# Optimization experiments

Measured on AMD Instinct MI355X. Metric: run time of the kernel, lower is better.

The kernel has to match this reference:

```python
import jax, jax.numpy as jnp
import numpy as np

N0 = 50000
N1 = 50000
E = 500000
IN_DIM = 128
OUT_DIM = 128
H = 8
DK = OUT_DIM // H  # 16
SQRT_DK = float(np.sqrt(DK))
NUM_TYPES = 2
NUM_REL = 3
# relations: (src_type, dst_type, e_id)
RELATIONS = [(0, 1, 0), (1, 0, 1), (0, 0, 2)]


def setup_inputs() -> dict:
    key = jax.random.key(0)
    ks = jax.random.split(key, 24)
    d = {}
    d["h0"] = jax.random.normal(ks[0], (N0, IN_DIM), dtype=jnp.float32)
    d["h1"] = jax.random.normal(ks[1], (N1, IN_DIM), dtype=jnp.float32)
    d["src0"] = jax.random.randint(ks[2], (E,), 0, N0)
    d["dst0"] = jax.random.randint(ks[3], (E,), 0, N1)
    d["src1"] = jax.random.randint(ks[4], (E,), 0, N1)
    d["dst1"] = jax.random.randint(ks[5], (E,), 0, N0)
    d["src2"] = jax.random.randint(ks[6], (E,), 0, N0)
    d["dst2"] = jax.random.randint(ks[7], (E,), 0, N0)
    w_scale = 1.0 / np.sqrt(IN_DIM)
    # per-node-type stacked linear weights (k, q, v, a), torch Linear convention: y = x @ W.T + b
    d["Wk"] = jax.random.normal(ks[8], (NUM_TYPES, OUT_DIM, IN_DIM), dtype=jnp.float32) * w_scale
    d["bk"] = jnp.zeros((NUM_TYPES, OUT_DIM), dtype=jnp.float32)
    d["Wq"] = jax.random.normal(ks[9], (NUM_TYPES, OUT_DIM, IN_DIM), dtype=jnp.float32) * w_scale
    d["bq"] = jnp.zeros((NUM_TYPES, OUT_DIM), dtype=jnp.float32)
    d["Wv"] = jax.random.normal(ks[10], (NUM_TYPES, OUT_DIM, IN_DIM), dtype=jnp.float32) * w_scale
    d["bv"] = jnp.zeros((NUM_TYPES, OUT_DIM), dtype=jnp.float32)
    d["Wa"] = jax.random.normal(ks[11], (NUM_TYPES, OUT_DIM, OUT_DIM), dtype=jnp.float32) * w_scale
    d["ba"] = jnp.zeros((NUM_TYPES, OUT_DIM), dtype=jnp.float32)
    xavier = float(np.sqrt(6.0 / (DK + DK)))
    d["rel_att"] = jax.random.uniform(ks[12], (NUM_REL, H, DK, DK), dtype=jnp.float32, minval=-xavier, maxval=xavier)
    d["rel_msg"] = jax.random.uniform(ks[13], (NUM_REL, H, DK, DK), dtype=jnp.float32, minval=-xavier, maxval=xavier)
    d["rel_pri"] = jnp.ones((NUM_REL, H), dtype=jnp.float32)
    d["skip"] = jnp.ones((NUM_TYPES,), dtype=jnp.float32)
    return d


def _lin(x, W, b):
    return x @ W.T + b


def reference(h0, h1, src0, dst0, src1, dst1, src2, dst2,
              Wk, bk, Wq, bq, Wv, bv, Wa, ba,
              rel_att, rel_msg, rel_pri, skip):
    h = [h0, h1]
    edges = [(src0, dst0), (src1, dst1), (src2, dst2)]
    # per-type projections, reshaped to (N, H, DK)
    k = [_lin(h[t], Wk[t], bk[t]).reshape(-1, H, DK) for t in range(NUM_TYPES)]
    q = [_lin(h[t], Wq[t], bq[t]).reshape(-1, H, DK) for t in range(NUM_TYPES)]
    v = [_lin(h[t], Wv[t], bv[t]).reshape(-1, H, DK) for t in range(NUM_TYPES)]

    agg = [[] for _ in range(NUM_TYPES)]
    for (s, dt, e), (src, dst) in zip(RELATIONS, edges):
        # relation-specific transforms of source k and v
        kr = jnp.einsum('nhi,hij->nhj', k[s], rel_att[e])
        vr = jnp.einsum('nhi,hij->nhj', v[s], rel_msg[e])
        # per-edge dot-product score (E, H)
        score = (q[dt][dst] * kr[src]).sum(-1) * rel_pri[e] / SQRT_DK
        n_dst = h[dt].shape[0]
        # edge softmax normalized by dst (stable)
        m = jax.ops.segment_max(score, dst, num_segments=n_dst)
        ex = jnp.exp(score - m[dst])
        den = jax.ops.segment_sum(ex, dst, num_segments=n_dst)
        attn = ex / den[dst]  # (E, H)
        # weighted message scatter-sum -> (n_dst, H, DK)
        msg = vr[src] * attn[:, :, None]
        agg[dt].append(jax.ops.segment_sum(msg, dst, num_segments=n_dst))

    new_h = []
    for t in range(NUM_TYPES):
        # cross_reducer='mean' over relations targeting this node type
        tmean = sum(agg[t]) / float(len(agg[t]))
        tflat = tmean.reshape(-1, OUT_DIM)
        trans = _lin(tflat, Wa[t], ba[t])  # dropout = identity (eval)
        alpha = jax.nn.sigmoid(skip[t])
        new_h.append(trans * alpha + h[t] * (1.0 - alpha))
    return tuple(new_h)
```

## Files before the change

### kernel.cpp

```cpp
#include <hip/hip_runtime.h>

typedef __attribute__((ext_vector_type(8))) _Float16 half8;
typedef __attribute__((ext_vector_type(2))) _Float16 half2v;
typedef __attribute__((ext_vector_type(4))) float f32x4;

#define NB 196
#define CHK 2048
#define CAPB 4096
#define PSTRIDE 6144

__device__ __forceinline__ unsigned short f2h(float f) {
  _Float16 h = (_Float16)f;
  return __builtin_bit_cast(unsigned short, h);
}
__device__ __forceinline__ float fdot2(unsigned a, unsigned b, float c) {
  return __builtin_amdgcn_fdot2(__builtin_bit_cast(half2v, a), __builtin_bit_cast(half2v, b), c,
                                false);
}

#define DPPADD(v, ctrl) \
  ((v) + __int_as_float(__builtin_amdgcn_update_dpp(0, __float_as_int(v), ctrl, 0xF, 0xF, true)))

__global__ void cvt2_kernel(const float* __restrict__ a, unsigned short* __restrict__ oa,
                            const float* __restrict__ b, unsigned short* __restrict__ ob,
                            int n8, unsigned short* __restrict__ z0,
                            unsigned short* __restrict__ z1, unsigned short* __restrict__ z2) {
  int t = threadIdx.x;
  if (blockIdx.y == 2) {
    if (blockIdx.x == 0 && t < 192) {
      int r = t >> 6;
      unsigned short* z = r == 0 ? z0 : (r == 1 ? z1 : z2);
      ((uint2*)z)[t & 63] = make_uint2(0, 0);
    }
    return;
  }
  int i = blockIdx.x * 256 + t;
  if (i >= n8) return;
  const float* in = blockIdx.y ? b : a;
  unsigned short* out = blockIdx.y ? ob : oa;
  const float4* p = (const float4*)(in + (size_t)i * 8);
  float4 x = p[0], y = p[1];
  uint4 v;
  v.x = f2h(x.x) | ((unsigned)f2h(x.y) << 16);
  v.y = f2h(x.z) | ((unsigned)f2h(x.w) << 16);
  v.z = f2h(y.x) | ((unsigned)f2h(y.y) << 16);
  v.w = f2h(y.z) | ((unsigned)f2h(y.w) << 16);
  *(uint4*)(out + (size_t)i * 8) = v;
}

__global__ void compose_w_kernel(const float* __restrict__ Wk, const float* __restrict__ bk,
                                 const float* __restrict__ Wv, const float* __restrict__ bv,
                                 const float* __restrict__ rel_att, const float* __restrict__ rel_msg,
                                 const float* __restrict__ rel_pri,
                                 unsigned short* __restrict__ Wkr, float* __restrict__ bkr,
                                 unsigned short* __restrict__ Wvr, float* __restrict__ bvr) {
  int e = blockIdx.x;
  int o = blockIdx.y;
  int z = blockIdx.z;
  int c = threadIdx.x;
  int hd = o >> 4, j = o & 15;
  const int se[3] = {0, 1, 0};
  int s = se[e];
  const float* W = z ? Wv : Wk;
  const float* b = z ? bv : bk;
  const float* R = z ? rel_msg : rel_att;
  float scale = z ? 1.0f : (rel_pri[e * 8 + hd] * 0.25f);
  float acc = 0.0f, bacc = 0.0f;
#pragma unroll
  for (int i = 0; i < 16; ++i) {
    float r = R[((e * 8 + hd) * 16 + i) * 16 + j];
    acc += W[(s * 128 + hd * 16 + i) * 128 + c] * r;
    bacc += b[s * 128 + hd * 16 + i] * r;
  }
  unsigned short* Wo = z ? Wvr : Wkr;
  float* bo = z ? bvr : bkr;
  Wo[((size_t)e * 128 + o) * 128 + c] = f2h(acc * scale);
  if (c == 0) bo[e * 128 + o] = bacc * scale;
}

struct ProjFP {
  const float* A[2];
  int M[2];
  int nj[2];
  const unsigned short* W[10];
  const float* b[10];
  unsigned short* out[10];
  int ostr[10];
};

__global__ __launch_bounds__(256) void proj_gemm_fused(ProjFP P) {
  __shared__ short As[128 * 128];
  int type = blockIdx.y;
  const float* __restrict__ A = P.A[type];
  int M = P.M[type];
  int nj = P.nj[type];
  int base = type * 5;
  int row0 = blockIdx.x * 128;
  if (row0 >= M) return;
  int t = threadIdx.x;
  bool full = (row0 + 128 <= M);
#pragma unroll
  for (int it = 0; it < 8; ++it) {
    int o = (it * 256 + t) * 8;
    int row = o >> 7, col = o & 127;
    int gr = row0 + row;
    uint4 av = make_uint4(0, 0, 0, 0);
    if (full || gr < M) {
      float4 x = *(const float4*)(A + (size_t)gr * 128 + col);
      float4 y = *(const float4*)(A + (size_t)gr * 128 + col + 4);
      av.x = f2h(x.x) | ((unsigned)f2h(x.y) << 16);
      av.y = f2h(x.z) | ((unsigned)f2h(x.w) << 16);
      av.z = f2h(y.x) | ((unsigned)f2h(y.y) << 16);
      av.w = f2h(y.z) | ((unsigned)f2h(y.w) << 16);
    }
    int sw = o ^ ((row & 7) << 3);
    *(uint4*)(&As[sw]) = av;
  }
  __syncthreads();
  int wid = t >> 6, l = t & 63;
  int wr = wid >> 1, wc = wid & 1;
  int lr = l & 15, kb = l >> 4;
  for (int j = 0;; ++j) {
    const unsigned short* __restrict__ W = P.W[base + j];
    f32x4 acc[4][4] = {};
#pragma unroll
    for (int ks = 0; ks < 4; ++ks) {
      half8 af[4], bfr[4];
#pragma unroll
      for (int m = 0; m < 4; ++m) {
        int row = wr * 64 + m * 16 + lr;
        int h = (row * 128 + kb * 8 + ks * 32) ^ ((row & 7) << 3);
        af[m] = *(half8*)(&As[h]);
      }
#pragma unroll
      for (int n = 0; n < 4; ++n) {
        int row = wc * 64 + n * 16 + lr;
        bfr[n] = *(const half8*)(W + (size_t)row * 128 + kb * 8 + ks * 32);
      }
#pragma unroll
      for (int m = 0; m < 4; ++m)
#pragma unroll
        for (int n = 0; n < 4; ++n)
          acc[m][n] = __builtin_amdgcn_mfma_f32_16x16x32_f16(af[m], bfr[n], acc[m][n], 0, 0, 0);
    }
    const float* bias = P.b[base + j];
    unsigned short* out = P.out[base + j];
    int ostr = P.ostr[base + j];
    int rb = row0 + wr * 64 + (l >> 4) * 4;
#pragma unroll
    for (int m = 0; m < 4; ++m)
#pragma unroll
      for (int jr = 0; jr < 4; ++jr) {
        int grow = rb + m * 16 + jr;
        if (grow < M) {
#pragma unroll
          for (int n = 0; n < 4; ++n) {
            int col = wc * 64 + n * 16 + lr;
            out[(size_t)grow * ostr + col] = f2h(acc[m][n][jr] + bias[col]);
          }
        }
      }
    if (j + 1 >= nj) break;
  }
}

__global__ __launch_bounds__(256) void final_gemm_mfma(
    float* __restrict__ dout, const unsigned short* __restrict__ Tb0,
    const unsigned short* __restrict__ Tb1, const unsigned short* __restrict__ Wab,
    const float* __restrict__ ba, const float* __restrict__ h0, const float* __restrict__ h1,
    const float* __restrict__ skip, int N0, int N1) {
  __shared__ short As[128 * 128];
  int type = blockIdx.y;
  int M = type ? N1 : N0;
  const unsigned short* T = type ? Tb1 : Tb0;
  const unsigned short* W = Wab + (size_t)type * 16384;
  const float* bias = ba + type * 128;
  const float* h = type ? h1 : h0;
  float* O = dout + (type ? (size_t)N0 * 128 : 0);
  int row0 = blockIdx.x * 128;
  if (row0 >= M) return;
  int t = threadIdx.x;
  bool full = (row0 + 128 <= M);
#pragma unroll
  for (int it = 0; it < 8; ++it) {
    int o = (it * 256 + t) * 8;
    int row = o >> 7;
    int gr = row0 + row;
    uint4 av = make_uint4(0, 0, 0, 0);
    if (full || gr < M) av = *(const uint4*)(T + (size_t)gr * 128 + (o & 127));
    int sw = o ^ ((row & 7) << 3);
    *(uint4*)(&As[sw]) = av;
  }
  __syncthreads();
  int wid = t >> 6, l = t & 63;
  int wr = wid >> 1, wc = wid & 1;
  int lr = l & 15, kb = l >> 4;
  f32x4 acc[4][4] = {};
#pragma unroll
  for (int ks = 0; ks < 4; ++ks) {
    half8 af[4], bfr[4];
#pragma unroll
    for (int m = 0; m < 4; ++m) {
      int row = wr * 64 + m * 16 + lr;
      int h2 = (row * 128 + kb * 8 + ks * 32) ^ ((row & 7) << 3);
      af[m] = *(half8*)(&As[h2]);
    }
#pragma unroll
    for (int n = 0; n < 4; ++n) {
      int row = wc * 64 + n * 16 + lr;
      bfr[n] = *(const half8*)(W + (size_t)row * 128 + kb * 8 + ks * 32);
    }
#pragma unroll
    for (int m = 0; m < 4; ++m)
#pragma unroll
      for (int n = 0; n < 4; ++n)
        acc[m][n] = __builtin_amdgcn_mfma_f32_16x16x32_f16(af[m], bfr[n], acc[m][n], 0, 0, 0);
  }
  float alpha = 1.0f / (1.0f + __expf(-skip[type]));
  float beta = 1.0f - alpha;
  int rb = row0 + wr * 64 + (l >> 4) * 4;
#pragma unroll
  for (int m = 0; m < 4; ++m)
#pragma unroll
    for (int jr = 0; jr < 4; ++jr) {
      int grow = rb + m * 16 + jr;
      if (grow < M) {
#pragma unroll
        for (int n = 0; n < 4; ++n) {
          int col = wc * 64 + n * 16 + lr;
          float vout = alpha * (acc[m][n][jr] + bias[col]) + beta * h[(size_t)grow * 128 + col];
          O[(size_t)grow * 128 + col] = vout;
        }
      }
    }
}


__global__ __launch_bounds__(256) void bhist_kernel(const int* __restrict__ d0,
                                                    const int* __restrict__ d1,
                                                    const int* __restrict__ d2,
                                                    int* __restrict__ bh, int E) {
  __shared__ int lh[NB];
  int r = blockIdx.y;
  const int* dst = r == 0 ? d0 : (r == 1 ? d1 : d2);
  int t = threadIdx.x;
  int lo = blockIdx.x * CHK;
  int hi = lo + CHK < E ? lo + CHK : E;
  for (int j = t; j < NB; j += 256) lh[j] = 0;
  __syncthreads();
  for (int i = lo + t; i < hi; i += 256) atomicAdd(&lh[dst[i] >> 8], 1);
  __syncthreads();
  for (int j = t; j < NB; j += 256) {
    int v = lh[j];
    if (v) atomicAdd(&bh[r * NB + j], v);
  }
}

__global__ __launch_bounds__(256) void bin_kernel(
    const int* __restrict__ s0, const int* __restrict__ d0, const int* __restrict__ s1,
    const int* __restrict__ d1, const int* __restrict__ s2, const int* __restrict__ d2,
    const int* __restrict__ bh, int* __restrict__ bcur, unsigned* __restrict__ bo0,
    unsigned* __restrict__ bo1, unsigned* __restrict__ bo2, int E) {
  __shared__ unsigned st[CHK];
  __shared__ int ga[CHK];
  __shared__ int hist[NB];
  __shared__ int scn[256];
  __shared__ int gb[NB];
  __shared__ int bbl[NB];
  int r = blockIdx.y;
  const int* src = r == 0 ? s0 : (r == 1 ? s1 : s2);
  const int* dst = r == 0 ? d0 : (r == 1 ? d1 : d2);
  unsigned* bo = r == 0 ? bo0 : (r == 1 ? bo1 : bo2);
  int t = threadIdx.x;
  {
    int v0 = (t < NB) ? bh[r * NB + t] : 0;
    scn[t] = v0;
    __syncthreads();
    for (int off = 1; off < 256; off <<= 1) {
      int u = (t >= off) ? scn[t - off] : 0;
      __syncthreads();
      scn[t] += u;
      __syncthreads();
    }
    if (t < NB) bbl[t] = scn[t] - v0;
    __syncthreads();
  }
  int lo = blockIdx.x * CHK;
  int hi = lo + CHK < E ? lo + CHK : E;
  int nloc = hi - lo;
  if (nloc <= 0) return;
  for (int j = t; j < NB; j += 256) hist[j] = 0;
  __syncthreads();
  int myb[CHK / 256], myr[CHK / 256];
  unsigned mye[CHK / 256];
#pragma unroll
  for (int k = 0; k < CHK / 256; ++k) {
    int i = lo + k * 256 + t;
    myb[k] = -1;
    if (i < hi) {
      int d = dst[i];
      int b = d >> 8;
      mye[k] = (unsigned)src[i] | ((unsigned)d << 16);
      myb[k] = b;
      myr[k] = atomicAdd(&hist[b], 1);
    }
  }
  __syncthreads();
  int v = (t < NB) ? hist[t] : 0;
  scn[t] = v;
  __syncthreads();
  for (int off = 1; off < 256; off <<= 1) {
    int u = (t >= off) ? scn[t - off] : 0;
    __syncthreads();
    scn[t] += u;
    __syncthreads();
  }
  int excl = scn[t] - v;
  __syncthreads();
  scn[t] = excl;
  if (t < NB && v > 0) gb[t] = atomicAdd(&bcur[r * NB + t], v);
  __syncthreads();
#pragma unroll
  for (int k = 0; k < CHK / 256; ++k) {
    if (myb[k] >= 0) {
      int slot = scn[myb[k]] + myr[k];
      st[slot] = mye[k];
      ga[slot] = bbl[myb[k]] + gb[myb[k]] + myr[k];
    }
  }
  __syncthreads();
  for (int j = t; j < nloc; j += 256) bo[ga[j]] = st[j];
}

__global__ __launch_bounds__(256) void bsort_kernel(
    const unsigned* __restrict__ bo0, const unsigned* __restrict__ bo1,
    const unsigned* __restrict__ bo2, const int* __restrict__ bh, int* __restrict__ rs0,
    int* __restrict__ rs1, int* __restrict__ rs2, int* __restrict__ re0, int* __restrict__ re1,
    int* __restrict__ re2, unsigned* __restrict__ sp0, unsigned* __restrict__ sp1,
    unsigned* __restrict__ sp2, int nd0, int nd1, int nd2, int ns0, int ns1, int ns2, int E) {
  __shared__ unsigned ed[CAPB];
  __shared__ unsigned srt[PSTRIDE];
  __shared__ unsigned short rank[CAPB];
  __shared__ int hist[256];
  __shared__ int scn[256];
  __shared__ int bbl[NB + 1];
  int r = blockIdx.y, b = blockIdx.x;
  const unsigned* bo = r == 0 ? bo0 : (r == 1 ? bo1 : bo2);
  int* rs = r == 0 ? rs0 : (r == 1 ? rs1 : rs2);
  int* re = r == 0 ? re0 : (r == 1 ? re1 : re2);
  unsigned* sp = r == 0 ? sp0 : (r == 1 ? sp1 : sp2);
  int nd = r == 0 ? nd0 : (r == 1 ? nd1 : nd2);
  unsigned sentinel = (unsigned)(r == 0 ? ns0 : (r == 1 ? ns1 : ns2));
  int t = threadIdx.x;
  {
    int v0 = (t < NB) ? bh[r * NB + t] : 0;
    scn[t] = v0;
    __syncthreads();
    for (int off = 1; off < 256; off <<= 1) {
      int u = (t >= off) ? scn[t - off] : 0;
      __syncthreads();
      scn[t] += u;
      __syncthreads();
    }
    if (t < NB) bbl[t] = scn[t] - v0;
    if (t == 0) bbl[NB] = E;
    __syncthreads();
  }
  int base = bbl[b], endb = bbl[b + 1];
  int cnt = endb - base;
  if (cnt > CAPB) cnt = CAPB;
  int nlo = b << 8;
  int nn = nd - nlo;
  if (nn > 256) nn = 256;
  if (nn < 0) nn = 0;
  hist[t] = 0;
  for (int j = t; j < cnt; j += 256) ed[j] = bo[base + j];
  __syncthreads();
  for (int j = t; j < cnt; j += 256) {
    int node = (ed[j] >> 16) & 255;
    rank[j] = (unsigned short)atomicAdd(&hist[node], 1);
  }
  __syncthreads();
  int rawh = hist[t];
  int pd = (rawh + 7) & ~7;
  scn[t] = pd;
  __syncthreads();
  for (int off = 1; off < 256; off <<= 1) {
    int u = (t >= off) ? scn[t - off] : 0;
    __syncthreads();
    scn[t] += u;
    __syncthreads();
  }
  int pexcl = scn[t] - pd;
  int ptot = scn[255];
  __syncthreads();
  hist[t] = pexcl;
  __syncthreads();
  if (t < nn) {
    rs[nlo + t] = b * PSTRIDE + pexcl;
    re[nlo + t] = b * PSTRIDE + pexcl + rawh;
  }
  int ptot32 = (ptot + 31) & ~31;
  for (int j = t; j < ptot32; j += 256) srt[j] = sentinel;
  __syncthreads();
  for (int j = t; j < cnt; j += 256) {
    int node = (ed[j] >> 16) & 255;
    srt[hist[node] + rank[j]] = ed[j];
  }
  __syncthreads();
  unsigned* spb = sp + (size_t)b * PSTRIDE;
  for (int j = t; j < ptot32; j += 256) spb[j] = srt[j];
}

struct FuP {
  const unsigned *sp0, *sp1, *sp2;
  const unsigned *kv0, *kv1, *kv2;
  const unsigned *qb0, *qb1;
  const int *rs0, *rs1, *rs2;
  const int *re0, *re1, *re2;
  unsigned *Tb0, *Tb1;
  int N0, N1;
};

__device__ __forceinline__ void loadRows(const char* __restrict__ kvlk,
                                         const char* __restrict__ kvlv, unsigned sv, int half,
                                         uint2 kf[4], uint2 vf[4]) {
#pragma unroll
  for (int g = 0; g < 4; ++g) {
    unsigned pA = __builtin_amdgcn_readlane(sv, g);
    unsigned pB = __builtin_amdgcn_readlane(sv, g + 4);
    unsigned pk = half ? pB : pA;
    size_t off = (size_t)(pk & 0xFFFFu) << 9;
    kf[g] = *(const uint2*)(kvlk + off);
    vf[g] = *(const uint2*)(kvlv + off);
  }
}

__device__ __forceinline__ void computeKV(const uint2 kf[4], const uint2 vf[4], unsigned qx,
                                          unsigned qy, float& a0, float& a1, float& a2,
                                          float& a3, float& den) {
#pragma unroll
  for (int g = 0; g < 4; ++g) {
    float sc = fdot2(kf[g].y, qy, fdot2(kf[g].x, qx, 0.f));
    sc = DPPADD(sc, 0xB1);
    sc = DPPADD(sc, 0x4E);
    float e = __expf(sc);
    den += e;
    unsigned eu = f2h(e);
    unsigned pl = eu;
    unsigned ph = eu << 16;
    a0 = fdot2(vf[g].x, pl, a0);
    a1 = fdot2(vf[g].x, ph, a1);
    a2 = fdot2(vf[g].y, pl, a2);
    a3 = fdot2(vf[g].y, ph, a3);
  }
}

__device__ __forceinline__ void fuse_rel(const unsigned* __restrict__ sp,
                                         const unsigned* __restrict__ kv,
                                         const int* __restrict__ rs, const int* __restrict__ re,
                                         int node, int ll, int half, unsigned qx, unsigned qy,
                                         float& r0, float& r1, float& r2, float& r3) {
  int beg = __builtin_amdgcn_readfirstlane(rs[node]);
  int rend = __builtin_amdgcn_readfirstlane(re[node]);
  int raw = rend - beg;
  if (raw <= 0) return;
  int pd = (raw + 7) & ~7;
  int end = beg + pd;
  float npad = (float)(pd - raw);
  const char* kvlk = (const char*)kv + ll * 8;
  const char* kvlv = (const char*)kv + 256 + ll * 8;
  float a0 = 0.f, a1 = 0.f, a2 = 0.f, a3 = 0.f, den = 0.f;
  uint2 ka[4], va[4], kb2[4], vb2[4];
  int lane7 = threadIdx.x & 7;
  int p = beg;
  unsigned svA = sp[p + lane7];
  loadRows(kvlk, kvlv, svA, half, ka, va);
  unsigned svB = sp[p + 8 + lane7];
  for (;;) {
    if (p + 8 < end) loadRows(kvlk, kvlv, svB, half, kb2, vb2);
    svA = sp[p + 16 + lane7];
    computeKV(ka, va, qx, qy, a0, a1, a2, a3, den);
    p += 8;
    if (p >= end) break;
    if (p + 8 < end) loadRows(kvlk, kvlv, svA, half, ka, va);
    svB = sp[p + 16 + lane7];
    computeKV(kb2, vb2, qx, qy, a0, a1, a2, a3, den);
    p += 8;
    if (p >= end) break;
  }
  den += __shfl_xor(den, 32);
  a0 += __shfl_xor(a0, 32);
  a1 += __shfl_xor(a1, 32);
  a2 += __shfl_xor(a2, 32);
  a3 += __shfl_xor(a3, 32);
  den -= npad;
  float inv = 1.0f / den;
  r0 = fmaf(a0, inv, r0);
  r1 = fmaf(a1, inv, r1);
  r2 = fmaf(a2, inv, r2);
  r3 = fmaf(a3, inv, r3);
}

__global__ __launch_bounds__(256) void fusedge_kernel(FuP P) {
  int gw = (blockIdx.x * 256 + threadIdx.x) >> 6;
  int l = threadIdx.x & 63;
  int ll = l & 31, half = l >> 5;
  if (gw < P.N0) {
    uint2 q = *(const uint2*)((const char*)P.qb0 + (size_t)gw * 256 + ll * 8);
    float r0 = 0.f, r1 = 0.f, r2 = 0.f, r3 = 0.f;
    fuse_rel(P.sp1, P.kv1, P.rs1, P.re1, gw, ll, half, q.x, q.y, r0, r1, r2, r3);
    fuse_rel(P.sp2, P.kv2, P.rs2, P.re2, gw, ll, half, q.x, q.y, r0, r1, r2, r3);
    if (half == 0) {
      uint2 o;
      o.x = f2h(r0 * 0.5f) | ((unsigned)f2h(r1 * 0.5f) << 16);
      o.y = f2h(r2 * 0.5f) | ((unsigned)f2h(r3 * 0.5f) << 16);
      *(uint2*)(P.Tb0 + (size_t)gw * 64 + 2 * ll) = o;
    }
  } else if (gw < P.N0 + P.N1) {
    int n = gw - P.N0;
    uint2 q = *(const uint2*)((const char*)P.qb1 + (size_t)n * 256 + ll * 8);
    float r0 = 0.f, r1 = 0.f, r2 = 0.f, r3 = 0.f;
    fuse_rel(P.sp0, P.kv0, P.rs0, P.re0, n, ll, half, q.x, q.y, r0, r1, r2, r3);
    if (half == 0) {
      uint2 o;
      o.x = f2h(r0) | ((unsigned)f2h(r1) << 16);
      o.y = f2h(r2) | ((unsigned)f2h(r3) << 16);
      *(uint2*)(P.Tb1 + (size_t)n * 64 + 2 * ll) = o;
    }
  }
}

extern "C" void kernel_launch(void* const* d_in, const int* in_sizes, int n_in,
                              void* d_out, int out_size, void* d_ws, size_t ws_size,
                              hipStream_t stream) {
  const float* h0 = (const float*)d_in[0];
  const float* h1 = (const float*)d_in[1];
  const int* srcs[3] = {(const int*)d_in[2], (const int*)d_in[4], (const int*)d_in[6]};
  const int* dsts[3] = {(const int*)d_in[3], (const int*)d_in[5], (const int*)d_in[7]};
  const float* Wk = (const float*)d_in[8];
  const float* bk = (const float*)d_in[9];
  const float* Wq = (const float*)d_in[10];
  const float* bq = (const float*)d_in[11];
  const float* Wv = (const float*)d_in[12];
  const float* bv = (const float*)d_in[13];
  const float* Wa = (const float*)d_in[14];
  const float* ba = (const float*)d_in[15];
  const float* rel_att = (const float*)d_in[16];
  const float* rel_msg = (const float*)d_in[17];
  const float* rel_pri = (const float*)d_in[18];
  const float* skip = (const float*)d_in[19];

  int N0 = in_sizes[0] / 128;
  int N1 = in_sizes[1] / 128;
  int E = in_sizes[2];
  int nsrc[3] = {N0, N1, N0};
  int ndst[3] = {N1, N0, N0};
  int maxN = N0 > N1 ? N0 : N1;

  char* base = (char*)d_ws;
  size_t off = 0;
  auto alloc = [&](size_t bytes) -> void* {
    void* p = base + off;
    off += (bytes + 255) & ~(size_t)255;
    return p;
  };

  unsigned short* qb0 = (unsigned short*)alloc((size_t)N0 * 128 * 2);
  unsigned short* qb1 = (unsigned short*)alloc((size_t)N1 * 128 * 2);
  unsigned short* kvb[3];
  for (int r = 0; r < 3; ++r) kvb[r] = (unsigned short*)alloc((size_t)(nsrc[r] + 1) * 256 * 2);
  unsigned short* Tb0 = (unsigned short*)alloc((size_t)N0 * 128 * 2);
  unsigned short* Tb1 = (unsigned short*)alloc((size_t)N1 * 128 * 2);
  unsigned short* Wkrb = (unsigned short*)alloc((size_t)3 * 16384 * 2);
  unsigned short* Wvrb = (unsigned short*)alloc((size_t)3 * 16384 * 2);
  unsigned short* Wqb = (unsigned short*)alloc((size_t)2 * 16384 * 2);
  unsigned short* Wab = (unsigned short*)alloc((size_t)2 * 16384 * 2);
  float* bkr = (float*)alloc(3 * 128 * 4);
  float* bvr = (float*)alloc(3 * 128 * 4);
  int* rp_s[3];
  int* rp_e[3];
  unsigned* spk[3];
  unsigned* bo[3];
  for (int r = 0; r < 3; ++r) {
    rp_s[r] = (int*)alloc((size_t)ndst[r] * 4);
    rp_e[r] = (int*)alloc((size_t)ndst[r] * 4);
    spk[r] = (unsigned*)alloc((size_t)NB * PSTRIDE * 4);
    bo[r] = (unsigned*)alloc((size_t)(E + 64) * 4);
  }
  int* bcnt = (int*)alloc((size_t)2 * 3 * NB * 4);
  int* bhist = bcnt;
  int* bcur = bcnt + 3 * NB;
  (void)ws_size;

  compose_w_kernel<<<dim3(3, 128, 2), 128, 0, stream>>>(Wk, bk, Wv, bv, rel_att, rel_msg,
                                                        rel_pri, Wkrb, bkr, Wvrb, bvr);
  cvt2_kernel<<<dim3(16, 3), 256, 0, stream>>>(Wq, Wqb, Wa, Wab, 4096,
                                               kvb[0] + (size_t)nsrc[0] * 256,
                                               kvb[1] + (size_t)nsrc[1] * 256,
                                               kvb[2] + (size_t)nsrc[2] * 256);

  ProjFP pf;
  pf.A[0] = h0; pf.A[1] = h1;
  pf.M[0] = N0; pf.M[1] = N1;
  pf.nj[0] = 5; pf.nj[1] = 3;
  pf.W[0] = Wqb;            pf.b[0] = bq;        pf.out[0] = qb0;          pf.ostr[0] = 128;
  pf.W[1] = Wkrb;           pf.b[1] = bkr;       pf.out[1] = kvb[0];       pf.ostr[1] = 256;
  pf.W[2] = Wkrb + 32768;   pf.b[2] = bkr + 256; pf.out[2] = kvb[2];       pf.ostr[2] = 256;
  pf.W[3] = Wvrb;           pf.b[3] = bvr;       pf.out[3] = kvb[0] + 128; pf.ostr[3] = 256;
  pf.W[4] = Wvrb + 32768;   pf.b[4] = bvr + 256; pf.out[4] = kvb[2] + 128; pf.ostr[4] = 256;
  pf.W[5] = Wqb + 16384;    pf.b[5] = bq + 128;  pf.out[5] = qb1;          pf.ostr[5] = 128;
  pf.W[6] = Wkrb + 16384;   pf.b[6] = bkr + 128; pf.out[6] = kvb[1];       pf.ostr[6] = 256;
  pf.W[7] = Wvrb + 16384;   pf.b[7] = bvr + 128; pf.out[7] = kvb[1] + 128; pf.ostr[7] = 256;
  pf.W[8] = Wqb; pf.b[8] = bq; pf.out[8] = qb0; pf.ostr[8] = 128;
  pf.W[9] = Wqb; pf.b[9] = bq; pf.out[9] = qb0; pf.ostr[9] = 128;
  proj_gemm_fused<<<dim3((maxN + 127) / 128, 2), 256, 0, stream>>>(pf);

  hipMemsetAsync(bcnt, 0, (size_t)2 * 3 * NB * 4, stream);
  bhist_kernel<<<dim3((E + CHK - 1) / CHK, 3), 256, 0, stream>>>(dsts[0], dsts[1], dsts[2],
                                                                 bhist, E);
  bin_kernel<<<dim3((E + CHK - 1) / CHK, 3), 256, 0, stream>>>(
      srcs[0], dsts[0], srcs[1], dsts[1], srcs[2], dsts[2], bhist, bcur, bo[0], bo[1], bo[2], E);
  bsort_kernel<<<dim3(NB, 3), 256, 0, stream>>>(
      bo[0], bo[1], bo[2], bhist, rp_s[0], rp_s[1], rp_s[2], rp_e[0], rp_e[1], rp_e[2],
      spk[0], spk[1], spk[2], ndst[0], ndst[1], ndst[2], nsrc[0], nsrc[1], nsrc[2], E);

  FuP fp2;
  fp2.sp0 = spk[0]; fp2.sp1 = spk[1]; fp2.sp2 = spk[2];
  fp2.kv0 = (const unsigned*)kvb[0]; fp2.kv1 = (const unsigned*)kvb[1];
  fp2.kv2 = (const unsigned*)kvb[2];
  fp2.qb0 = (const unsigned*)qb0; fp2.qb1 = (const unsigned*)qb1;
  fp2.rs0 = rp_s[0]; fp2.rs1 = rp_s[1]; fp2.rs2 = rp_s[2];
  fp2.re0 = rp_e[0]; fp2.re1 = rp_e[1]; fp2.re2 = rp_e[2];
  fp2.Tb0 = (unsigned*)Tb0; fp2.Tb1 = (unsigned*)Tb1;
  fp2.N0 = N0; fp2.N1 = N1;
  int totw = N0 + N1;
  fusedge_kernel<<<(totw + 3) / 4, 256, 0, stream>>>(fp2);

  final_gemm_mfma<<<dim3((maxN + 127) / 128, 2), 256, 0, stream>>>(
      (float*)d_out, Tb0, Tb1, Wab, ba, h0, h1, skip, N0, N1);
}
```

Baseline: 252.9 us.

## Fuse bucket histogram into projection GEMM and stage weights in LDS

```diff
diff --git a/kernel.cpp b/kernel.cpp
--- a/kernel.cpp
+++ b/kernel.cpp
@@ -86,10 +86,33 @@
   const float* b[10];
   unsigned short* out[10];
   int ostr[10];
+  const int* dst[3];
+  int* bh;
+  int E;
 };
 
-__global__ __launch_bounds__(256) void proj_gemm_fused(ProjFP P) {
+__global__ __launch_bounds__(256) void proj_bhist_kernel(ProjFP P) {
   __shared__ short As[128 * 128];
+  __shared__ short Bs[128 * 128];
+  __shared__ int lh[NB];
+  int t = threadIdx.x;
+  if (blockIdx.y >= 2) {
+    int r = blockIdx.y - 2;
+    int nbh = (P.E + CHK - 1) / CHK;
+    if (blockIdx.x >= nbh) return;
+    const int* dst = P.dst[r];
+    int lo = blockIdx.x * CHK;
+    int hi = lo + CHK < P.E ? lo + CHK : P.E;
+    for (int j = t; j < NB; j += 256) lh[j] = 0;
+    __syncthreads();
+    for (int i = lo + t; i < hi; i += 256) atomicAdd(&lh[dst[i] >> 8], 1);
+    __syncthreads();
+    for (int j = t; j < NB; j += 256) {
+      int v = lh[j];
+      if (v) atomicAdd(&P.bh[r * NB + j], v);
+    }
+    return;
+  }
   int type = blockIdx.y;
   const float* __restrict__ A = P.A[type];
   int M = P.M[type];
@@ -97,7 +120,6 @@
   int base = type * 5;
   int row0 = blockIdx.x * 128;
   if (row0 >= M) return;
-  int t = threadIdx.x;
   bool full = (row0 + 128 <= M);
 #pragma unroll
   for (int it = 0; it < 8; ++it) {
@@ -116,12 +138,21 @@
     int sw = o ^ ((row & 7) << 3);
     *(uint4*)(&As[sw]) = av;
   }
+  {
+    const unsigned short* W0 = P.W[base];
+#pragma unroll
+    for (int it = 0; it < 8; ++it) {
+      int o = (it * 256 + t) * 8;
+      int row = o >> 7;
+      int sw = o ^ ((row & 7) << 3);
+      *(uint4*)(&Bs[sw]) = *(const uint4*)(W0 + o);
+    }
+  }
   __syncthreads();
   int wid = t >> 6, l = t & 63;
   int wr = wid >> 1, wc = wid & 1;
   int lr = l & 15, kb = l >> 4;
   for (int j = 0;; ++j) {
-    const unsigned short* __restrict__ W = P.W[base + j];
     f32x4 acc[4][4] = {};
 #pragma unroll
     for (int ks = 0; ks < 4; ++ks) {
@@ -135,7 +166,8 @@
 #pragma unroll
       for (int n = 0; n < 4; ++n) {
         int row = wc * 64 + n * 16 + lr;
-        bfr[n] = *(const half8*)(W + (size_t)row * 128 + kb * 8 + ks * 32);
+        int h = (row * 128 + kb * 8 + ks * 32) ^ ((row & 7) << 3);
+        bfr[n] = *(half8*)(&Bs[h]);
       }
 #pragma unroll
       for (int m = 0; m < 4; ++m)
@@ -161,6 +193,18 @@
         }
       }
     if (j + 1 >= nj) break;
+    __syncthreads();
+    {
+      const unsigned short* Wj = P.W[base + j + 1];
+#pragma unroll
+      for (int it = 0; it < 8; ++it) {
+        int o = (it * 256 + t) * 8;
+        int row = o >> 7;
+        int sw = o ^ ((row & 7) << 3);
+        *(uint4*)(&Bs[sw]) = *(const uint4*)(Wj + o);
+      }
+    }
+    __syncthreads();
   }
 }
 
@@ -170,6 +214,7 @@
     const float* __restrict__ ba, const float* __restrict__ h0, const float* __restrict__ h1,
     const float* __restrict__ skip, int N0, int N1) {
   __shared__ short As[128 * 128];
+  __shared__ short Bs[128 * 128];
   int type = blockIdx.y;
   int M = type ? N1 : N0;
   const unsigned short* T = type ? Tb1 : Tb0;
@@ -190,6 +235,8 @@
     if (full || gr < M) av = *(const uint4*)(T + (size_t)gr * 128 + (o & 127));
     int sw = o ^ ((row & 7) << 3);
     *(uint4*)(&As[sw]) = av;
+    uint4 wv = *(const uint4*)(W + o);
+    *(uint4*)(&Bs[sw]) = wv;
   }
   __syncthreads();
   int wid = t >> 6, l = t & 63;
@@ -208,7 +255,8 @@
 #pragma unroll
     for (int n = 0; n < 4; ++n) {
       int row = wc * 64 + n * 16 + lr;
-      bfr[n] = *(const half8*)(W + (size_t)row * 128 + kb * 8 + ks * 32);
+      int h2 = (row * 128 + kb * 8 + ks * 32) ^ ((row & 7) << 3);
+      bfr[n] = *(half8*)(&Bs[h2]);
     }
 #pragma unroll
     for (int m = 0; m < 4; ++m)
@@ -235,26 +283,6 @@
     }
 }
 
-
-__global__ __launch_bounds__(256) void bhist_kernel(const int* __restrict__ d0,
-                                                    const int* __restrict__ d1,
-                                                    const int* __restrict__ d2,
-                                                    int* __restrict__ bh, int E) {
-  __shared__ int lh[NB];
-  int r = blockIdx.y;
-  const int* dst = r == 0 ? d0 : (r == 1 ? d1 : d2);
-  int t = threadIdx.x;
-  int lo = blockIdx.x * CHK;
-  int hi = lo + CHK < E ? lo + CHK : E;
-  for (int j = t; j < NB; j += 256) lh[j] = 0;
-  __syncthreads();
-  for (int i = lo + t; i < hi; i += 256) atomicAdd(&lh[dst[i] >> 8], 1);
-  __syncthreads();
-  for (int j = t; j < NB; j += 256) {
-    int v = lh[j];
-    if (v) atomicAdd(&bh[r * NB + j], v);
-  }
-}
 
 __global__ __launch_bounds__(256) void bin_kernel(
     const int* __restrict__ s0, const int* __restrict__ d0, const int* __restrict__ s1,
@@ -422,17 +450,18 @@
   int N0, N1;
 };
 
-__device__ __forceinline__ void loadRows(const char* __restrict__ kvlk,
-                                         const char* __restrict__ kvlv, unsigned sv, int half,
-                                         uint2 kf[4], uint2 vf[4]) {
+__device__ __forceinline__ void loadKV(const char* __restrict__ kvl,
+                                       const unsigned* __restrict__ sp, int p, int half,
+                                       uint2 kf[4], uint2 vf[4]) {
+  unsigned sv = sp[p + (threadIdx.x & 7)];
 #pragma unroll
   for (int g = 0; g < 4; ++g) {
     unsigned pA = __builtin_amdgcn_readlane(sv, g);
     unsigned pB = __builtin_amdgcn_readlane(sv, g + 4);
     unsigned pk = half ? pB : pA;
-    size_t off = (size_t)(pk & 0xFFFFu) << 9;
-    kf[g] = *(const uint2*)(kvlk + off);
-    vf[g] = *(const uint2*)(kvlv + off);
+    const char* row = kvl + ((size_t)(pk & 0xFFFFu) << 9);
+    kf[g] = *(const uint2*)row;
+    vf[g] = *(const uint2*)(row + 256);
   }
 }
 
@@ -468,23 +497,17 @@
   int pd = (raw + 7) & ~7;
   int end = beg + pd;
   float npad = (float)(pd - raw);
-  const char* kvlk = (const char*)kv + ll * 8;
-  const char* kvlv = (const char*)kv + 256 + ll * 8;
+  const char* kvl = (const char*)kv + ll * 8;
   float a0 = 0.f, a1 = 0.f, a2 = 0.f, a3 = 0.f, den = 0.f;
   uint2 ka[4], va[4], kb2[4], vb2[4];
-  int lane7 = threadIdx.x & 7;
   int p = beg;
-  unsigned svA = sp[p + lane7];
-  loadRows(kvlk, kvlv, svA, half, ka, va);
-  unsigned svB = sp[p + 8 + lane7];
+  loadKV(kvl, sp, p, half, ka, va);
   for (;;) {
-    if (p + 8 < end) loadRows(kvlk, kvlv, svB, half, kb2, vb2);
-    svA = sp[p + 16 + lane7];
+    if (p + 8 < end) loadKV(kvl, sp, p + 8, half, kb2, vb2);
     computeKV(ka, va, qx, qy, a0, a1, a2, a3, den);
     p += 8;
     if (p >= end) break;
-    if (p + 8 < end) loadRows(kvlk, kvlv, svA, half, ka, va);
-    svB = sp[p + 16 + lane7];
+    if (p + 8 < end) loadKV(kvl, sp, p + 8, half, ka, va);
     computeKV(kb2, vb2, qx, qy, a0, a1, a2, a3, den);
     p += 8;
     if (p >= end) break;
@@ -593,6 +616,8 @@
   int* bcur = bcnt + 3 * NB;
   (void)ws_size;
 
+  hipMemsetAsync(bcnt, 0, (size_t)2 * 3 * NB * 4, stream);
+
   compose_w_kernel<<<dim3(3, 128, 2), 128, 0, stream>>>(Wk, bk, Wv, bv, rel_att, rel_msg,
                                                         rel_pri, Wkrb, bkr, Wvrb, bvr);
   cvt2_kernel<<<dim3(16, 3), 256, 0, stream>>>(Wq, Wqb, Wa, Wab, 4096,
@@ -614,11 +639,11 @@
   pf.W[7] = Wvrb + 16384;   pf.b[7] = bvr + 128; pf.out[7] = kvb[1] + 128; pf.ostr[7] = 256;
   pf.W[8] = Wqb; pf.b[8] = bq; pf.out[8] = qb0; pf.ostr[8] = 128;
   pf.W[9] = Wqb; pf.b[9] = bq; pf.out[9] = qb0; pf.ostr[9] = 128;
-  proj_gemm_fused<<<dim3((maxN + 127) / 128, 2), 256, 0, stream>>>(pf);
-
-  hipMemsetAsync(bcnt, 0, (size_t)2 * 3 * NB * 4, stream);
-  bhist_kernel<<<dim3((E + CHK - 1) / CHK, 3), 256, 0, stream>>>(dsts[0], dsts[1], dsts[2],
-                                                                 bhist, E);
+  pf.dst[0] = dsts[0]; pf.dst[1] = dsts[1]; pf.dst[2] = dsts[2];
+  pf.bh = bhist;
+  pf.E = E;
+  proj_bhist_kernel<<<dim3((maxN + 127) / 128, 5), 256, 0, stream>>>(pf);
+
   bin_kernel<<<dim3((E + CHK - 1) / CHK, 3), 256, 0, stream>>>(
       srcs[0], dsts[0], srcs[1], dsts[1], srcs[2], dsts[2], bhist, bcur, bo[0], bo[1], bo[2], E);
   bsort_kernel<<<dim3(NB, 3), 256, 0, stream>>>(
```

New measurement: 226.2 us. 1.12x faster.
